# Kernel tuning notes

Hardware: AMD Instinct MI355X
Metric: run time of the kernel (lower is better)

## Reference

```python
import jax, jax.numpy as jnp
import numpy as np
from jax import lax

N, G, L, D, E, STEPS = 65536, 128, 512, 128, 262144, 6
C = 2 * D  # concat dim (input_dim + output_dim)


def setup_inputs() -> dict:
    key = jax.random.key(0)
    ks = jax.random.split(key, 12)
    sD = 1.0 / float(np.sqrt(D))
    sC = 1.0 / float(np.sqrt(C))
    return {
        "x": jax.random.normal(ks[0], (N, D), jnp.float32),
        "edge_index": jax.random.randint(ks[1], (2, E), 0, N, dtype=jnp.int32),
        "edge_weight": jax.random.uniform(ks[2], (E,), jnp.float32),
        "batch": (jnp.arange(N) // L).astype(jnp.int32),  # sorted graph ids, L nodes/graph
        "ggnn_w": jax.random.normal(ks[3], (STEPS, D, D), jnp.float32) * sD,
        "gru_wih": jax.random.normal(ks[4], (3 * D, D), jnp.float32) * sD,
        "gru_whh": jax.random.normal(ks[5], (3 * D, D), jnp.float32) * sD,
        "gru_bih": jnp.zeros((3 * D,), jnp.float32),
        "gru_bhh": jnp.zeros((3 * D,), jnp.float32),
        "conv1_w": jax.random.normal(ks[6], (D, D, 3), jnp.float32) * sD,
        "conv1_b": jnp.zeros((D,), jnp.float32),
        "conv2_w": jax.random.normal(ks[7], (D, D, 1), jnp.float32) * sD,
        "conv2_b": jnp.zeros((D,), jnp.float32),
        "convc1_w": jax.random.normal(ks[8], (C, C, 3), jnp.float32) * sC,
        "convc1_b": jnp.zeros((C,), jnp.float32),
        "convc2_w": jax.random.normal(ks[9], (C, C, 1), jnp.float32) * sC,
        "convc2_b": jnp.zeros((C,), jnp.float32),
        "bn1_g": jnp.ones((D,), jnp.float32),
        "bn1_b": jnp.zeros((D,), jnp.float32),
        "bn2_g": jnp.ones((C,), jnp.float32),
        "bn2_b": jnp.zeros((C,), jnp.float32),
        "mlpy_w": jax.random.normal(ks[10], (2, D), jnp.float32) * sD,
        "mlpy_b": jnp.zeros((2,), jnp.float32),
        "mlpz_w": jax.random.normal(ks[11], (2, C), jnp.float32) * sC,
        "mlpz_b": jnp.zeros((2,), jnp.float32),
    }


def _gru(m, h, wih, whh, bih, bhh):
    gx = m @ wih.T + bih
    gh = h @ whh.T + bhh
    xr, xz, xn = jnp.split(gx, 3, axis=-1)
    hr, hz, hn = jnp.split(gh, 3, axis=-1)
    r = jax.nn.sigmoid(xr + hr)
    z = jax.nn.sigmoid(xz + hz)
    n = jnp.tanh(xn + r * hn)
    return (1.0 - z) * n + z * h


def _conv1d(x, w, b):  # x [G,Cin,L], w [Cout,Cin,K]
    y = lax.conv_general_dilated(x, w, (1,), "VALID", dimension_numbers=("NCH", "OIH", "NCH"))
    return y + b[None, :, None]


def _maxpool(x, k, s):
    return lax.reduce_window(x, -jnp.inf, lax.max, (1, 1, k), (1, 1, s), "VALID")


def _bn(x, g, b):  # training-mode BatchNorm1d over (N, L) per channel
    mean = x.mean(axis=(0, 2), keepdims=True)
    var = x.var(axis=(0, 2), keepdims=True)
    return (x - mean) * lax.rsqrt(var + 1e-5) * g[None, :, None] + b[None, :, None]


def reference(x, edge_index, edge_weight, batch, ggnn_w, gru_wih, gru_whh, gru_bih,
              gru_bhh, conv1_w, conv1_b, conv2_w, conv2_b, convc1_w, convc1_b,
              convc2_w, convc2_b, bn1_g, bn1_b, bn2_g, bn2_b, mlpy_w, mlpy_b,
              mlpz_w, mlpz_b):
    src, dst = edge_index[0], edge_index[1]

    # GatedGraphConv: per layer linear -> weighted message scatter-add -> GRU update
    def step(h, w):
        m = h @ w
        agg = jax.ops.segment_sum(m[src] * edge_weight[:, None], dst, num_segments=N)
        return _gru(agg, h, gru_wih, gru_whh, gru_bih, gru_bhh), None

    h, _ = lax.scan(step, x, ggnn_w)

    # de_batchify_graphs: one fused scatter into zero-padded [G, L, *] tensor
    counts = jax.ops.segment_sum(jnp.ones((N,), jnp.int32), batch, num_segments=G)
    offsets = jnp.cumsum(counts) - counts
    pos = jnp.arange(N) - offsets[batch]
    x_i = jnp.zeros((G, L, D), x.dtype).at[batch, pos].set(x)
    h_i = jnp.zeros((G, L, D), h.dtype).at[batch, pos].set(h)
    c_i = jnp.concatenate([h_i, x_i], axis=-1)  # [G, L, 2D]

    hT = h_i.transpose(0, 2, 1)  # [G, D, L]
    Y1 = _maxpool(jax.nn.relu(_bn(_conv1d(hT, conv1_w, conv1_b), bn1_g, bn1_b)), 3, 2)
    Y2 = _maxpool(jax.nn.relu(_bn(_conv1d(Y1, conv2_w, conv2_b), bn1_g, bn1_b)), 2, 2).transpose(0, 2, 1)
    cT = c_i.transpose(0, 2, 1)  # [G, 2D, L]
    Z1 = _maxpool(jax.nn.relu(_bn(_conv1d(cT, convc1_w, convc1_b), bn2_g, bn2_b)), 3, 2)
    Z2 = _maxpool(jax.nn.relu(_bn(_conv1d(Z1, convc2_w, convc2_b), bn2_g, bn2_b)), 2, 2).transpose(0, 2, 1)

    before_avg = (Y2 @ mlpy_w.T + mlpy_b) * (Z2 @ mlpz_w.T + mlpz_b)  # [G, L', 2]
    return before_avg.mean(axis=1)  # [G, 2]
```

## Files before the change

### kernel.cpp

```cpp
#include <hip/hip_runtime.h>
#include <math.h>

#define NN 65536
#define GG 128
#define LL 512
#define DD 128
#define EE 262144
#define NSTEPS 6
#define CC 256
#define L1 510
#define P1 254
#define P2 127

typedef __attribute__((ext_vector_type(8))) short s8bf;
typedef __attribute__((ext_vector_type(4))) float f4acc;

__device__ __forceinline__ unsigned short f2bf(float x) {
  unsigned u = __float_as_uint(x);
  unsigned r = u + 0x7FFFu + ((u >> 16) & 1u);
  return (unsigned short)(r >> 16);
}
__device__ __forceinline__ float bf2f(unsigned short h) {
  return __uint_as_float(((unsigned)h) << 16);
}
__device__ __forceinline__ unsigned short f2bf_sel(float x, int lo_sel) {
  unsigned short hi = f2bf(x);
  if (!lo_sel) return hi;
  return f2bf(x - bf2f(hi));
}
__device__ __forceinline__ uint2 pack4bf(float4 v, int lo_sel) {
  unsigned short s0 = f2bf_sel(v.x, lo_sel), s1 = f2bf_sel(v.y, lo_sel);
  unsigned short s2 = f2bf_sel(v.z, lo_sel), s3 = f2bf_sel(v.w, lo_sel);
  uint2 pk; pk.x = (unsigned)s0 | ((unsigned)s1 << 16);
  pk.y = (unsigned)s2 | ((unsigned)s3 << 16);
  return pk;
}

__global__ __launch_bounds__(256) void k_prep(
    const float* __restrict__ wih, const float* __restrict__ whh,
    const float* __restrict__ gw,
    const float* __restrict__ w1, const float* __restrict__ wc1,
    const float* __restrict__ w2, const float* __restrict__ wc2,
    unsigned short* __restrict__ wihCh, unsigned short* __restrict__ wihCl,
    unsigned short* __restrict__ whhCh, unsigned short* __restrict__ whhCl,
    unsigned short* __restrict__ gwTh, unsigned short* __restrict__ gwTl,
    unsigned short* __restrict__ c1h, unsigned short* __restrict__ c1l,
    unsigned short* __restrict__ cc1h, unsigned short* __restrict__ cc1l,
    unsigned short* __restrict__ c2h, unsigned short* __restrict__ c2l,
    unsigned short* __restrict__ cc2h, unsigned short* __restrict__ cc2l) {
  int i = blockIdx.x * 256 + threadIdx.x;
  if (i < 49152) {
    float v = wih[i];
    unsigned short h_ = f2bf(v);
    wihCh[i] = h_; wihCl[i] = f2bf(v - bf2f(h_));
    float u = whh[i];
    unsigned short h2 = f2bf(u);
    whhCh[i] = h2; whhCl[i] = f2bf(u - bf2f(h2));
  }
  if (i < 98304) {
    int s = i >> 14; int r = i & 16383; int c = r >> 7; int k = r & 127;
    float v = gw[(s << 14) + k * 128 + c];
    unsigned short h_ = f2bf(v);
    gwTh[i] = h_; gwTl[i] = f2bf(v - bf2f(h_));
  }
  if (i < 49152) {
    int ci = i & 127; int r = i >> 7; int co = r & 127; int tap = r >> 7;
    float v = w1[(co * 128 + ci) * 3 + tap];
    unsigned short h_ = f2bf(v);
    c1h[i] = h_; c1l[i] = f2bf(v - bf2f(h_));
  }
  if (i < 196608) {
    int ci = i & 255; int r = i >> 8; int co = r & 255; int tap = r >> 8;
    float v = wc1[(co * 256 + ci) * 3 + tap];
    unsigned short h_ = f2bf(v);
    cc1h[i] = h_; cc1l[i] = f2bf(v - bf2f(h_));
  }
  if (i < 16384) {
    float v = w2[i];
    unsigned short h_ = f2bf(v);
    c2h[i] = h_; c2l[i] = f2bf(v - bf2f(h_));
  }
  if (i < 65536) {
    float v = wc2[i];
    unsigned short h_ = f2bf(v);
    cc2h[i] = h_; cc2l[i] = f2bf(v - bf2f(h_));
  }
}

__global__ __launch_bounds__(256) void k_hist(const int* __restrict__ dst, int* __restrict__ cnt) {
  int e = blockIdx.x * 256 + threadIdx.x;
  if (e < EE) atomicAdd(&cnt[dst[e]], 1);
}

__global__ __launch_bounds__(1024) void k_scan(const int* __restrict__ cnt,
                                               int* __restrict__ rowptr,
                                               int* __restrict__ cursor) {
  __shared__ int part[1024];
  int t = threadIdx.x;
  int base = t * 64;
  int s = 0;
  for (int i = 0; i < 64; i++) s += cnt[base + i];
  part[t] = s;
  __syncthreads();
  for (int off = 1; off < 1024; off <<= 1) {
    int v = part[t];
    int u = (t >= off) ? part[t - off] : 0;
    __syncthreads();
    part[t] = v + u;
    __syncthreads();
  }
  int run = part[t] - s;
  for (int i = 0; i < 64; i++) {
    rowptr[base + i] = run;
    cursor[base + i] = run;
    run += cnt[base + i];
  }
  if (t == 1023) rowptr[NN] = run;
}

__global__ __launch_bounds__(256) void k_fill(const int* __restrict__ src,
                                              const int* __restrict__ dst,
                                              const float* __restrict__ ew,
                                              int* __restrict__ cursor,
                                              int* __restrict__ col,
                                              float* __restrict__ wgt) {
  int e = blockIdx.x * 256 + threadIdx.x;
  if (e < EE) {
    int d = dst[e];
    int p = atomicAdd(&cursor[d], 1);
    col[p] = src[e];
    wgt[p] = ew[e];
  }
}

__global__ __launch_bounds__(256, 4) void k_gemm_mfma(
    const float* __restrict__ A,
    const unsigned short* __restrict__ Wh, const unsigned short* __restrict__ Wl,
    float* __restrict__ Cout) {
  __shared__ __attribute__((aligned(16))) unsigned short As[64 * 136];
  int t = threadIdx.x;
  int r0 = blockIdx.x * 64;
  int wv = t >> 6, lane = t & 63;
  int ln = lane & 15, q = lane >> 4;
  f4acc acc[4][2];
#pragma unroll
  for (int mt = 0; mt < 4; mt++)
#pragma unroll
    for (int nt = 0; nt < 2; nt++) acc[mt][nt] = (f4acc)0.f;

  for (int p = 0; p < 3; p++) {
    if (p != 1) {
      const int a_lo = (p == 2);
      if (p) __syncthreads();
      for (int base = t * 4; base < 64 * 128; base += 1024) {
        int row = base >> 7, kk = base & 127;
        float4 v = *(const float4*)&A[(r0 + row) * 128 + kk];
        *(uint2*)&As[row * 136 + kk] = pack4bf(v, a_lo);
      }
      __syncthreads();
    }
    const unsigned short* W = (p == 1) ? Wl : Wh;
#pragma unroll
    for (int k0 = 0; k0 < 128; k0 += 32) {
      s8bf af[4], bf[2];
#pragma unroll
      for (int nt = 0; nt < 2; nt++)
        bf[nt] = *(const s8bf*)&W[(wv * 32 + nt * 16 + ln) * 128 + k0 + q * 8];
#pragma unroll
      for (int mt = 0; mt < 4; mt++)
        af[mt] = *(const s8bf*)&As[(mt * 16 + ln) * 136 + k0 + q * 8];
#pragma unroll
      for (int mt = 0; mt < 4; mt++)
#pragma unroll
        for (int nt = 0; nt < 2; nt++)
          acc[mt][nt] = __builtin_amdgcn_mfma_f32_16x16x32_bf16(af[mt], bf[nt], acc[mt][nt], 0, 0, 0);
    }
  }
#pragma unroll
  for (int mt = 0; mt < 4; mt++)
#pragma unroll
    for (int nt = 0; nt < 2; nt++)
#pragma unroll
      for (int reg = 0; reg < 4; reg++) {
        int r = r0 + mt * 16 + q * 4 + reg;
        Cout[r * 128 + wv * 32 + nt * 16 + ln] = acc[mt][nt][reg];
      }
}

__global__ __launch_bounds__(256) void k_gather(const float* __restrict__ m,
                                                const int* __restrict__ rowptr,
                                                const int* __restrict__ col,
                                                const float* __restrict__ wgt,
                                                float* __restrict__ agg) {
  int t = threadIdx.x;
  int n = blockIdx.x * 8 + (t >> 5);
  int c4 = t & 31;
  const float4* m4 = (const float4*)m;
  int s0 = rowptr[n], s1 = rowptr[n + 1];
  float ax = 0.f, ay = 0.f, az = 0.f, aw = 0.f;
  int e = s0;
  for (; e + 2 <= s1; e += 2) {
    int cA = col[e], cB = col[e + 1];
    float wA = wgt[e], wB = wgt[e + 1];
    float4 vA = m4[cA * 32 + c4];
    float4 vB = m4[cB * 32 + c4];
    ax += vA.x * wA + vB.x * wB;
    ay += vA.y * wA + vB.y * wB;
    az += vA.z * wA + vB.z * wB;
    aw += vA.w * wA + vB.w * wB;
  }
  if (e < s1) {
    int cA = col[e];
    float wA = wgt[e];
    float4 vA = m4[cA * 32 + c4];
    ax += vA.x * wA; ay += vA.y * wA; az += vA.z * wA; aw += vA.w * wA;
  }
  ((float4*)agg)[n * 32 + c4] = make_float4(ax, ay, az, aw);
}

__global__ __launch_bounds__(256, 2) void k_gru_mfma(
    const float* __restrict__ agg, const float* __restrict__ hin,
    const unsigned short* __restrict__ wihCh, const unsigned short* __restrict__ wihCl,
    const unsigned short* __restrict__ whhCh, const unsigned short* __restrict__ whhCl,
    const float* __restrict__ bih, const float* __restrict__ bhh,
    float* __restrict__ hout) {
  __shared__ __attribute__((aligned(16))) unsigned short As[2 * 64 * 136];
  int t = threadIdx.x;
  int r0 = blockIdx.x * 64;
  int d0 = blockIdx.y * 64;
  int wv = t >> 6, lane = t & 63;
  int ln = lane & 15, q = lane >> 4;
  f4acc acc[4][6];
#pragma unroll
  for (int mt = 0; mt < 4; mt++)
#pragma unroll
    for (int tg = 0; tg < 6; tg++) acc[mt][tg] = (f4acc)0.f;

  for (int p = 0; p < 3; p++) {
    if (p != 1) {
      const int a_lo = (p == 2);
      if (p) __syncthreads();
#pragma unroll
      for (int mat = 0; mat < 2; mat++) {
        const float* Asrc = mat ? hin : agg;
        for (int base = t * 4; base < 64 * 128; base += 1024) {
          int row = base >> 7, kk = base & 127;
          float4 v = *(const float4*)&Asrc[(r0 + row) * 128 + kk];
          *(uint2*)&As[mat * 8704 + row * 136 + kk] = pack4bf(v, a_lo);
        }
      }
      __syncthreads();
    }
    const unsigned short* wx = (p == 1) ? wihCl : wihCh;
    const unsigned short* wh = (p == 1) ? whhCl : whhCh;
#pragma unroll
    for (int k0 = 0; k0 < 128; k0 += 32) {
      s8bf af[2][4], bfr[6];
#pragma unroll
      for (int tg = 0; tg < 6; tg++) {
        int gate = (tg < 3) ? tg : tg - 3;
        const unsigned short* W = (tg < 3) ? wx : wh;
        bfr[tg] = *(const s8bf*)&W[(gate * 128 + d0 + wv * 16 + ln) * 128 + k0 + q * 8];
      }
#pragma unroll
      for (int mat = 0; mat < 2; mat++)
#pragma unroll
        for (int mt = 0; mt < 4; mt++)
          af[mat][mt] = *(const s8bf*)&As[mat * 8704 + (mt * 16 + ln) * 136 + k0 + q * 8];
#pragma unroll
      for (int mt = 0; mt < 4; mt++)
#pragma unroll
        for (int tg = 0; tg < 6; tg++)
          acc[mt][tg] = __builtin_amdgcn_mfma_f32_16x16x32_bf16(
              af[tg < 3 ? 0 : 1][mt], bfr[tg], acc[mt][tg], 0, 0, 0);
    }
  }
  int d = d0 + wv * 16 + ln;
  float bi0 = bih[d], bi1 = bih[128 + d], bi2 = bih[256 + d];
  float bh0 = bhh[d], bh1 = bhh[128 + d], bh2 = bhh[256 + d];
#pragma unroll
  for (int mt = 0; mt < 4; mt++) {
#pragma unroll
    for (int reg = 0; reg < 4; reg++) {
      int r = r0 + mt * 16 + q * 4 + reg;
      float hold = hin[r * 128 + d];
      float xr = acc[mt][0][reg] + bi0;
      float xz = acc[mt][1][reg] + bi1;
      float xn = acc[mt][2][reg] + bi2;
      float hr = acc[mt][3][reg] + bh0;
      float hz = acc[mt][4][reg] + bh1;
      float hn = acc[mt][5][reg] + bh2;
      float rr = 1.f / (1.f + expf(-(xr + hr)));
      float zz = 1.f / (1.f + expf(-(xz + hz)));
      float nnv = tanhf(xn + rr * hn);
      hout[r * 128 + d] = (1.f - zz) * nnv + zz * hold;
    }
  }
}

template<int CIN, int TAPS, int WA>
__global__ __launch_bounds__(256, 3) void k_conv_mfma(
    const float* __restrict__ inA, const float* __restrict__ inB,
    const unsigned short* __restrict__ Wh, const unsigned short* __restrict__ Wl,
    const float* __restrict__ bias, float* __restrict__ out,
    float* __restrict__ stats, int Lin, int Lco) {
  constexpr int APAD = CIN + 8;
  constexpr int ROWS = 64 + TAPS - 1;
  constexpr int NCH = CIN / 32;
  __shared__ __attribute__((aligned(16))) unsigned short As[ROWS * APAD];
  __shared__ float sred[256];
  const int g = blockIdx.z, co0 = blockIdx.y * 128, l0 = blockIdx.x * 64;
  const int t = threadIdx.x;
  const int wv = t >> 6, lane = t & 63, ln = lane & 15, q = lane >> 4;
  f4acc acc[4][2];
#pragma unroll
  for (int mt = 0; mt < 4; mt++)
#pragma unroll
    for (int nt = 0; nt < 2; nt++) acc[mt][nt] = (f4acc)0.f;

  for (int p = 0; p < 3; p++) {
    if (p != 1) {
      const int a_lo = (p == 2);
      if (p) __syncthreads();
      for (int base = t * 4; base < ROWS * CIN; base += 1024) {
        int row = base / CIN, ch = base % CIN;
        int lr = l0 + row; if (lr > Lin - 1) lr = Lin - 1;
        float4 v;
        if (ch < WA) v = *(const float4*)&inA[(g * Lin + lr) * WA + ch];
        else         v = *(const float4*)&inB[(g * Lin + lr) * WA + ch - WA];
        *(uint2*)&As[row * APAD + ch] = pack4bf(v, a_lo);
      }
      __syncthreads();
    }
    const unsigned short* W = (p == 1) ? Wl : Wh;
#pragma unroll
    for (int tap = 0; tap < TAPS; tap++) {
#pragma unroll
      for (int ch = 0; ch < NCH; ch++) {
        const int c0 = ch * 32;
        s8bf af[4], bf[2];
#pragma unroll
        for (int nt = 0; nt < 2; nt++)
          bf[nt] = *(const s8bf*)&W[(tap * CIN + co0 + wv * 32 + nt * 16 + ln) * CIN + c0 + q * 8];
#pragma unroll
        for (int mt = 0; mt < 4; mt++)
          af[mt] = *(const s8bf*)&As[(mt * 16 + ln + tap) * APAD + c0 + q * 8];
#pragma unroll
        for (int mt = 0; mt < 4; mt++)
#pragma unroll
          for (int nt = 0; nt < 2; nt++)
            acc[mt][nt] = __builtin_amdgcn_mfma_f32_16x16x32_bf16(af[mt], bf[nt], acc[mt][nt], 0, 0, 0);
      }
    }
  }
  sred[t] = 0.f;
  __syncthreads();
#pragma unroll
  for (int nt = 0; nt < 2; nt++) {
    int cl = wv * 32 + nt * 16 + ln;
    int co = co0 + cl;
    float bv = bias[co];
    float s = 0.f, s2 = 0.f;
#pragma unroll
    for (int mt = 0; mt < 4; mt++)
#pragma unroll
      for (int reg = 0; reg < 4; reg++) {
        int l = l0 + mt * 16 + q * 4 + reg;
        if (l < Lco) {
          float v = acc[mt][nt][reg] + bv;
          out[(g * Lco + l) * CIN + co] = v;
          s += v; s2 += v * v;
        }
      }
    atomicAdd(&sred[cl], s);
    atomicAdd(&sred[128 + cl], s2);
  }
  __syncthreads();
  if (t < 128) atomicAdd(&stats[co0 + t], sred[t]);
  else atomicAdd(&stats[CIN + co0 + (t - 128)], sred[t]);
}

__global__ __launch_bounds__(256) void k_bnpool(const float* __restrict__ in,
                                                float* __restrict__ out,
                                                const float* __restrict__ stats,
                                                const float* __restrict__ gamma,
                                                const float* __restrict__ beta,
                                                int Cch, int LinC, int Lout, int pk) {
  int idx = blockIdx.x * 256 + threadIdx.x;
  int total = GG * Cch * Lout;
  if (idx >= total) return;
  int c = idx & (Cch - 1);
  int r = idx / Cch;
  int p = r % Lout;
  int g = r / Lout;
  float cntf = (float)(GG * LinC);
  float mean = stats[c] / cntf;
  float var = stats[Cch + c] / cntf - mean * mean;
  float inv = rsqrtf(var + 1e-5f) * gamma[c];
  float sh = beta[c] - mean * inv;
  const float* base = &in[((g * LinC) + 2 * p) * Cch + c];
  float m = 0.f;
  for (int k = 0; k < pk; k++) {
    float v = fmaxf(base[k * Cch] * inv + sh, 0.f);
    m = fmaxf(m, v);
  }
  out[(g * Lout + p) * Cch + c] = m;
}

__global__ __launch_bounds__(128) void k_final(const float* __restrict__ Y2,
                                               const float* __restrict__ Z2,
                                               const float* __restrict__ myw,
                                               const float* __restrict__ myb,
                                               const float* __restrict__ mzw,
                                               const float* __restrict__ mzb,
                                               float* __restrict__ outp) {
  __shared__ float red0[128];
  __shared__ float red1[128];
  int g = blockIdx.x;
  int t = threadIdx.x;
  float y0 = myb[0], y1 = myb[1], z0 = mzb[0], z1 = mzb[1];
  if (t < P2) {
    const float* yb = &Y2[(g * P2 + t) * 128];
    for (int c = 0; c < 128; c++) {
      float v = yb[c];
      y0 += v * myw[c];
      y1 += v * myw[128 + c];
    }
    const float* zb = &Z2[(g * P2 + t) * 256];
    for (int c = 0; c < 256; c++) {
      float v = zb[c];
      z0 += v * mzw[c];
      z1 += v * mzw[256 + c];
    }
  }
  red0[t] = (t < P2) ? y0 * z0 : 0.f;
  red1[t] = (t < P2) ? y1 * z1 : 0.f;
  __syncthreads();
  for (int off = 64; off > 0; off >>= 1) {
    if (t < off) {
      red0[t] += red0[t + off];
      red1[t] += red1[t + off];
    }
    __syncthreads();
  }
  if (t == 0) {
    outp[g * 2 + 0] = red0[0] / 127.f;
    outp[g * 2 + 1] = red1[0] / 127.f;
  }
}

extern "C" void kernel_launch(void* const* d_in, const int* in_sizes, int n_in,
                              void* d_out, int out_size, void* d_ws, size_t ws_size,
                              hipStream_t stream) {
  const float* x   = (const float*)d_in[0];
  const int* ei    = (const int*)d_in[1];
  const float* ew  = (const float*)d_in[2];
  const float* gw  = (const float*)d_in[4];
  const float* wih = (const float*)d_in[5];
  const float* whh = (const float*)d_in[6];
  const float* bih = (const float*)d_in[7];
  const float* bhh = (const float*)d_in[8];
  const float* w1  = (const float*)d_in[9];
  const float* b1  = (const float*)d_in[10];
  const float* w2  = (const float*)d_in[11];
  const float* b2  = (const float*)d_in[12];
  const float* wc1 = (const float*)d_in[13];
  const float* bc1 = (const float*)d_in[14];
  const float* wc2 = (const float*)d_in[15];
  const float* bc2 = (const float*)d_in[16];
  const float* bn1g = (const float*)d_in[17];
  const float* bn1b = (const float*)d_in[18];
  const float* bn2g = (const float*)d_in[19];
  const float* bn2b = (const float*)d_in[20];
  const float* myw = (const float*)d_in[21];
  const float* myb = (const float*)d_in[22];
  const float* mzw = (const float*)d_in[23];
  const float* mzb = (const float*)d_in[24];
  float* out = (float*)d_out;

  float* ws   = (float*)d_ws;
  float* h    = ws;
  float* bufA = h + 8388608;
  float* bufB = bufA + 16711680;
  float* bufC = bufB + 8388608;
  float* Y2   = bufC + 8388608;
  float* Z2   = Y2 + 2080768;
  float* wslot = Z2 + 4161536;
  unsigned short* wihCh = (unsigned short*)wslot;
  unsigned short* wihCl = wihCh + 49152;
  unsigned short* whhCh = wihCl + 49152;
  unsigned short* whhCl = whhCh + 49152;
  unsigned short* c1h  = (unsigned short*)(wslot + 98304);
  unsigned short* c1l  = c1h + 49152;
  unsigned short* cc1h = c1l + 49152;
  unsigned short* cc1l = cc1h + 196608;
  unsigned short* c2h  = cc1l + 196608;
  unsigned short* c2l  = c2h + 16384;
  unsigned short* cc2h = c2l + 16384;
  unsigned short* cc2l = cc2h + 65536;
  float* stats = (float*)(cc2l + 65536);
  int* cnt    = (int*)(stats + 512);
  int* rowptr = cnt + 65536;
  int* cursor = rowptr + 65537;
  int* col    = cursor + 65536;
  float* wgt  = (float*)(col + 262144);
  unsigned short* gwTh = (unsigned short*)(wgt + 262144);
  unsigned short* gwTl = gwTh + 98304;
  size_t needed = (size_t)((float*)(gwTl + 98304) - ws) * 4;
  if (ws_size < needed) return;

  const int* src = ei;
  const int* dst = ei + EE;

  k_prep<<<768, 256, 0, stream>>>(wih, whh, gw, w1, wc1, w2, wc2,
                                  wihCh, wihCl, whhCh, whhCl, gwTh, gwTl,
                                  c1h, c1l, cc1h, cc1l, c2h, c2l, cc2h, cc2l);
  hipMemsetAsync(cnt, 0, 65536 * 4, stream);
  k_hist<<<1024, 256, 0, stream>>>(dst, cnt);
  k_scan<<<1, 1024, 0, stream>>>(cnt, rowptr, cursor);
  k_fill<<<1024, 256, 0, stream>>>(src, dst, ew, cursor, col, wgt);

  float* P = h;
  float* Q = bufC;
  float* m = bufA;
  float* agg = bufB;
  for (int s = 0; s < NSTEPS; s++) {
    const float* hcur = (s == 0) ? x : ((s & 1) ? Q : P);
    float* hnext = (s & 1) ? P : Q;
    k_gemm_mfma<<<1024, 256, 0, stream>>>(hcur, gwTh + s * 16384, gwTl + s * 16384, m);
    k_gather<<<8192, 256, 0, stream>>>(m, rowptr, col, wgt, agg);
    k_gru_mfma<<<dim3(1024, 2), 256, 0, stream>>>(agg, hcur, wihCh, wihCl,
                                                  whhCh, whhCl, bih, bhh, hnext);
  }

  hipMemsetAsync(stats, 0, 512 * 4, stream);
  k_conv_mfma<128, 3, 128><<<dim3(8, 1, 128), 256, 0, stream>>>(
      h, nullptr, c1h, c1l, b1, bufA, stats, 512, L1);
  k_bnpool<<<(GG * 128 * P1 + 255) / 256, 256, 0, stream>>>(bufA, bufB, stats, bn1g, bn1b, 128, L1, P1, 3);
  hipMemsetAsync(stats, 0, 512 * 4, stream);
  k_conv_mfma<128, 1, 128><<<dim3(4, 1, 128), 256, 0, stream>>>(
      bufB, nullptr, c2h, c2l, b2, bufC, stats, P1, P1);
  k_bnpool<<<(GG * 128 * P2 + 255) / 256, 256, 0, stream>>>(bufC, Y2, stats, bn1g, bn1b, 128, P1, P2, 2);

  hipMemsetAsync(stats, 0, 512 * 4, stream);
  k_conv_mfma<256, 3, 128><<<dim3(8, 2, 128), 256, 0, stream>>>(
      h, x, cc1h, cc1l, bc1, bufA, stats, 512, L1);
  k_bnpool<<<(GG * 256 * P1 + 255) / 256, 256, 0, stream>>>(bufA, bufB, stats, bn2g, bn2b, 256, L1, P1, 3);
  hipMemsetAsync(stats, 0, 512 * 4, stream);
  k_conv_mfma<256, 1, 256><<<dim3(4, 2, 128), 256, 0, stream>>>(
      bufB, nullptr, cc2h, cc2l, bc2, bufC, stats, P1, P1);
  k_bnpool<<<(GG * 256 * P2 + 255) / 256, 256, 0, stream>>>(bufC, Z2, stats, bn2g, bn2b, 256, P1, P2, 2);

  k_final<<<128, 128, 0, stream>>>(Y2, Z2, myw, myb, mzw, mzb, out);
}
```

Before: 1.648 ms.

## Store activations as split bf16 hi/lo planes instead of fp32 across pipeline

```diff
diff --git a/kernel.cpp b/kernel.cpp
--- a/kernel.cpp
+++ b/kernel.cpp
@@ -87,6 +87,21 @@
   }
 }
 
+__global__ __launch_bounds__(256) void k_castx(const float* __restrict__ x,
+                                               unsigned short* __restrict__ xH,
+                                               unsigned short* __restrict__ xL) {
+  int i = blockIdx.x * 256 + threadIdx.x;
+  const float4* x4 = (const float4*)x;
+  float4 a = x4[i * 2 + 0];
+  float4 b = x4[i * 2 + 1];
+  uint2 ha = pack4bf(a, 0), hb = pack4bf(b, 0);
+  uint2 la = pack4bf(a, 1), lb = pack4bf(b, 1);
+  uint4 hv; hv.x = ha.x; hv.y = ha.y; hv.z = hb.x; hv.w = hb.y;
+  uint4 lv; lv.x = la.x; lv.y = la.y; lv.z = lb.x; lv.w = lb.y;
+  *(uint4*)&xH[i * 8] = hv;
+  *(uint4*)&xL[i * 8] = lv;
+}
+
 __global__ __launch_bounds__(256) void k_hist(const int* __restrict__ dst, int* __restrict__ cnt) {
   int e = blockIdx.x * 256 + threadIdx.x;
   if (e < EE) atomicAdd(&cnt[dst[e]], 1);
@@ -134,7 +149,7 @@
 }
 
 __global__ __launch_bounds__(256, 4) void k_gemm_mfma(
-    const float* __restrict__ A,
+    const unsigned short* __restrict__ Ah, const unsigned short* __restrict__ Al,
     const unsigned short* __restrict__ Wh, const unsigned short* __restrict__ Wl,
     float* __restrict__ Cout) {
   __shared__ __attribute__((aligned(16))) unsigned short As[64 * 136];
@@ -150,12 +165,13 @@
 
   for (int p = 0; p < 3; p++) {
     if (p != 1) {
-      const int a_lo = (p == 2);
+      const unsigned short* S = (p == 2) ? Al : Ah;
       if (p) __syncthreads();
-      for (int base = t * 4; base < 64 * 128; base += 1024) {
-        int row = base >> 7, kk = base & 127;
-        float4 v = *(const float4*)&A[(r0 + row) * 128 + kk];
-        *(uint2*)&As[row * 136 + kk] = pack4bf(v, a_lo);
+#pragma unroll
+      for (int it = 0; it < 4; it++) {
+        int v8 = it * 256 + t;
+        int row = v8 >> 4, k = (v8 & 15) * 8;
+        *(uint4*)&As[row * 136 + k] = *(const uint4*)&S[(r0 + row) * 128 + k];
       }
       __syncthreads();
     }
@@ -191,7 +207,8 @@
                                                 const int* __restrict__ rowptr,
                                                 const int* __restrict__ col,
                                                 const float* __restrict__ wgt,
-                                                float* __restrict__ agg) {
+                                                unsigned short* __restrict__ aggH,
+                                                unsigned short* __restrict__ aggL) {
   int t = threadIdx.x;
   int n = blockIdx.x * 8 + (t >> 5);
   int c4 = t & 31;
@@ -215,15 +232,24 @@
     float4 vA = m4[cA * 32 + c4];
     ax += vA.x * wA; ay += vA.y * wA; az += vA.z * wA; aw += vA.w * wA;
   }
-  ((float4*)agg)[n * 32 + c4] = make_float4(ax, ay, az, aw);
+  unsigned short h0 = f2bf(ax), h1 = f2bf(ay), h2 = f2bf(az), h3 = f2bf(aw);
+  unsigned short l0 = f2bf(ax - bf2f(h0)), l1 = f2bf(ay - bf2f(h1));
+  unsigned short l2 = f2bf(az - bf2f(h2)), l3 = f2bf(aw - bf2f(h3));
+  uint2 hpk, lpk;
+  hpk.x = (unsigned)h0 | ((unsigned)h1 << 16); hpk.y = (unsigned)h2 | ((unsigned)h3 << 16);
+  lpk.x = (unsigned)l0 | ((unsigned)l1 << 16); lpk.y = (unsigned)l2 | ((unsigned)l3 << 16);
+  int base = n * 128 + c4 * 4;
+  *(uint2*)&aggH[base] = hpk;
+  *(uint2*)&aggL[base] = lpk;
 }
 
 __global__ __launch_bounds__(256, 2) void k_gru_mfma(
-    const float* __restrict__ agg, const float* __restrict__ hin,
+    const unsigned short* __restrict__ aggH, const unsigned short* __restrict__ aggL,
+    const unsigned short* __restrict__ hinH, const unsigned short* __restrict__ hinL,
     const unsigned short* __restrict__ wihCh, const unsigned short* __restrict__ wihCl,
     const unsigned short* __restrict__ whhCh, const unsigned short* __restrict__ whhCl,
     const float* __restrict__ bih, const float* __restrict__ bhh,
-    float* __restrict__ hout) {
+    unsigned short* __restrict__ houtH, unsigned short* __restrict__ houtL) {
   __shared__ __attribute__((aligned(16))) unsigned short As[2 * 64 * 136];
   int t = threadIdx.x;
   int r0 = blockIdx.x * 64;
@@ -238,16 +264,16 @@
 
   for (int p = 0; p < 3; p++) {
     if (p != 1) {
-      const int a_lo = (p == 2);
+      const unsigned short* s0 = (p == 2) ? aggL : aggH;
+      const unsigned short* s1 = (p == 2) ? hinL : hinH;
       if (p) __syncthreads();
 #pragma unroll
-      for (int mat = 0; mat < 2; mat++) {
-        const float* Asrc = mat ? hin : agg;
-        for (int base = t * 4; base < 64 * 128; base += 1024) {
-          int row = base >> 7, kk = base & 127;
-          float4 v = *(const float4*)&Asrc[(r0 + row) * 128 + kk];
-          *(uint2*)&As[mat * 8704 + row * 136 + kk] = pack4bf(v, a_lo);
-        }
+      for (int it = 0; it < 8; it++) {
+        int v8 = it * 256 + t;
+        int mat = v8 >> 10;
+        int row = (v8 >> 4) & 63, k = (v8 & 15) * 8;
+        const unsigned short* S = mat ? s1 : s0;
+        *(uint4*)&As[mat * 8704 + row * 136 + k] = *(const uint4*)&S[(r0 + row) * 128 + k];
       }
       __syncthreads();
     }
@@ -283,7 +309,8 @@
 #pragma unroll
     for (int reg = 0; reg < 4; reg++) {
       int r = r0 + mt * 16 + q * 4 + reg;
-      float hold = hin[r * 128 + d];
+      int idx = r * 128 + d;
+      float hold = bf2f(hinH[idx]) + bf2f(hinL[idx]);
       float xr = acc[mt][0][reg] + bi0;
       float xz = acc[mt][1][reg] + bi1;
       float xn = acc[mt][2][reg] + bi2;
@@ -293,20 +320,27 @@
       float rr = 1.f / (1.f + expf(-(xr + hr)));
       float zz = 1.f / (1.f + expf(-(xz + hz)));
       float nnv = tanhf(xn + rr * hn);
-      hout[r * 128 + d] = (1.f - zz) * nnv + zz * hold;
+      float hv = (1.f - zz) * nnv + zz * hold;
+      unsigned short hh = f2bf(hv);
+      houtH[idx] = hh;
+      houtL[idx] = f2bf(hv - bf2f(hh));
     }
   }
 }
 
 template<int CIN, int TAPS, int WA>
-__global__ __launch_bounds__(256, 3) void k_conv_mfma(
-    const float* __restrict__ inA, const float* __restrict__ inB,
+__global__ __launch_bounds__(256, 4) void k_conv_mfma(
+    const unsigned short* __restrict__ hiA, const unsigned short* __restrict__ hiB,
+    const unsigned short* __restrict__ loA, const unsigned short* __restrict__ loB,
     const unsigned short* __restrict__ Wh, const unsigned short* __restrict__ Wl,
     const float* __restrict__ bias, float* __restrict__ out,
     float* __restrict__ stats, int Lin, int Lco) {
   constexpr int APAD = CIN + 8;
   constexpr int ROWS = 64 + TAPS - 1;
   constexpr int NCH = CIN / 32;
+  constexpr int TOT8 = ROWS * CIN / 8;
+  constexpr int NIT = (TOT8 + 255) / 256;
+  constexpr int NINNER = TAPS * NCH;
   __shared__ __attribute__((aligned(16))) unsigned short As[ROWS * APAD];
   __shared__ float sred[256];
   const int g = blockIdx.z, co0 = blockIdx.y * 128, l0 = blockIdx.x * 64;
@@ -320,37 +354,48 @@
 
   for (int p = 0; p < 3; p++) {
     if (p != 1) {
-      const int a_lo = (p == 2);
+      const unsigned short* pA = (p == 2) ? loA : hiA;
+      const unsigned short* pB = (p == 2) ? loB : hiB;
       if (p) __syncthreads();
-      for (int base = t * 4; base < ROWS * CIN; base += 1024) {
-        int row = base / CIN, ch = base % CIN;
-        int lr = l0 + row; if (lr > Lin - 1) lr = Lin - 1;
-        float4 v;
-        if (ch < WA) v = *(const float4*)&inA[(g * Lin + lr) * WA + ch];
-        else         v = *(const float4*)&inB[(g * Lin + lr) * WA + ch - WA];
-        *(uint2*)&As[row * APAD + ch] = pack4bf(v, a_lo);
+#pragma unroll
+      for (int it = 0; it < NIT; it++) {
+        int v8 = it * 256 + t;
+        if (NIT * 256 == TOT8 || v8 < TOT8) {
+          int row = (v8 * 8) / CIN, ch = (v8 * 8) % CIN;
+          int lr = l0 + row; if (lr > Lin - 1) lr = Lin - 1;
+          uint4 v;
+          if (ch < WA) v = *(const uint4*)&pA[(g * Lin + lr) * WA + ch];
+          else         v = *(const uint4*)&pB[(g * Lin + lr) * WA + ch - WA];
+          *(uint4*)&As[row * APAD + ch] = v;
+        }
       }
       __syncthreads();
     }
     const unsigned short* W = (p == 1) ? Wl : Wh;
-#pragma unroll
-    for (int tap = 0; tap < TAPS; tap++) {
-#pragma unroll
-      for (int ch = 0; ch < NCH; ch++) {
-        const int c0 = ch * 32;
-        s8bf af[4], bf[2];
+    s8bf bcur[2], bnxt[2];
+#pragma unroll
+    for (int nt = 0; nt < 2; nt++)
+      bcur[nt] = *(const s8bf*)&W[(co0 + wv * 32 + nt * 16 + ln) * CIN + q * 8];
+#pragma unroll
+    for (int it = 0; it < NINNER; it++) {
+      const int tap = it / NCH, ch = it % NCH;
+      if (it + 1 < NINNER) {
+        const int ntap = (it + 1) / NCH, nch = (it + 1) % NCH;
 #pragma unroll
         for (int nt = 0; nt < 2; nt++)
-          bf[nt] = *(const s8bf*)&W[(tap * CIN + co0 + wv * 32 + nt * 16 + ln) * CIN + c0 + q * 8];
-#pragma unroll
-        for (int mt = 0; mt < 4; mt++)
-          af[mt] = *(const s8bf*)&As[(mt * 16 + ln + tap) * APAD + c0 + q * 8];
-#pragma unroll
-        for (int mt = 0; mt < 4; mt++)
-#pragma unroll
-          for (int nt = 0; nt < 2; nt++)
-            acc[mt][nt] = __builtin_amdgcn_mfma_f32_16x16x32_bf16(af[mt], bf[nt], acc[mt][nt], 0, 0, 0);
+          bnxt[nt] = *(const s8bf*)&W[(ntap * CIN + co0 + wv * 32 + nt * 16 + ln) * CIN + nch * 32 + q * 8];
       }
+      const int c0 = ch * 32;
+      s8bf af[4];
+#pragma unroll
+      for (int mt = 0; mt < 4; mt++)
+        af[mt] = *(const s8bf*)&As[(mt * 16 + ln + tap) * APAD + c0 + q * 8];
+#pragma unroll
+      for (int mt = 0; mt < 4; mt++)
+#pragma unroll
+        for (int nt = 0; nt < 2; nt++)
+          acc[mt][nt] = __builtin_amdgcn_mfma_f32_16x16x32_bf16(af[mt], bcur[nt], acc[mt][nt], 0, 0, 0);
+      if (it + 1 < NINNER) { bcur[0] = bnxt[0]; bcur[1] = bnxt[1]; }
     }
   }
   sred[t] = 0.f;
@@ -380,8 +425,11 @@
   else atomicAdd(&stats[CIN + co0 + (t - 128)], sred[t]);
 }
 
+template<bool PLANES>
 __global__ __launch_bounds__(256) void k_bnpool(const float* __restrict__ in,
-                                                float* __restrict__ out,
+                                                float* __restrict__ outF,
+                                                unsigned short* __restrict__ outH,
+                                                unsigned short* __restrict__ outL,
                                                 const float* __restrict__ stats,
                                                 const float* __restrict__ gamma,
                                                 const float* __restrict__ beta,
@@ -404,7 +452,14 @@
     float v = fmaxf(base[k * Cch] * inv + sh, 0.f);
     m = fmaxf(m, v);
   }
-  out[(g * Lout + p) * Cch + c] = m;
+  int o = (g * Lout + p) * Cch + c;
+  if (PLANES) {
+    unsigned short hh = f2bf(m);
+    outH[o] = hh;
+    outL[o] = f2bf(m - bf2f(hh));
+  } else {
+    outF[o] = m;
+  }
 }
 
 __global__ __launch_bounds__(128) void k_final(const float* __restrict__ Y2,
@@ -478,19 +533,12 @@
   const float* mzb = (const float*)d_in[24];
   float* out = (float*)d_out;
 
-  float* ws   = (float*)d_ws;
-  float* h    = ws;
-  float* bufA = h + 8388608;
-  float* bufB = bufA + 16711680;
-  float* bufC = bufB + 8388608;
-  float* Y2   = bufC + 8388608;
-  float* Z2   = Y2 + 2080768;
-  float* wslot = Z2 + 4161536;
-  unsigned short* wihCh = (unsigned short*)wslot;
-  unsigned short* wihCl = wihCh + 49152;
-  unsigned short* whhCh = wihCl + 49152;
-  unsigned short* whhCl = whhCh + 49152;
-  unsigned short* c1h  = (unsigned short*)(wslot + 98304);
+  float* ws = (float*)d_ws;
+  unsigned short* PH = (unsigned short*)ws;
+  unsigned short* PL = PH + 8388608;
+  unsigned short* xH = PL + 8388608;
+  unsigned short* xL = xH + 8388608;
+  unsigned short* c1h  = xL + 8388608;
   unsigned short* c1l  = c1h + 49152;
   unsigned short* cc1h = c1l + 49152;
   unsigned short* cc1l = cc1h + 196608;
@@ -499,14 +547,32 @@
   unsigned short* cc2h = c2l + 16384;
   unsigned short* cc2l = cc2h + 65536;
   float* stats = (float*)(cc2l + 65536);
-  int* cnt    = (int*)(stats + 512);
+  float* Y2 = stats + 512;
+  float* Z2 = Y2 + 2080768;
+  float* shared0 = Z2 + 4161536;
+  unsigned short* QH = (unsigned short*)shared0;
+  unsigned short* QL = QH + 8388608;
+  float* m = (float*)(QL + 8388608);
+  unsigned short* aggH = (unsigned short*)(m + 8388608);
+  unsigned short* aggL = aggH + 8388608;
+  unsigned short* wihCh = aggL + 8388608;
+  unsigned short* wihCl = wihCh + 49152;
+  unsigned short* whhCh = wihCl + 49152;
+  unsigned short* whhCl = whhCh + 49152;
+  unsigned short* gwTh = whhCl + 49152;
+  unsigned short* gwTl = gwTh + 98304;
+  int* cnt    = (int*)(gwTl + 98304);
   int* rowptr = cnt + 65536;
   int* cursor = rowptr + 65537;
   int* col    = cursor + 65536;
   float* wgt  = (float*)(col + 262144);
-  unsigned short* gwTh = (unsigned short*)(wgt + 262144);
-  unsigned short* gwTl = gwTh + 98304;
-  size_t needed = (size_t)((float*)(gwTl + 98304) - ws) * 4;
+  float* ggnn_end = wgt + 262144;
+  float* bufA = shared0;
+  unsigned short* bufBH = (unsigned short*)(bufA + 16711680);
+  unsigned short* bufBL = bufBH + 8323072;
+  float* conv_end = (float*)(bufBL + 8323072);
+  float* wend = (ggnn_end > conv_end) ? ggnn_end : conv_end;
+  size_t needed = (size_t)(wend - ws) * 4;
   if (ws_size < needed) return;
 
   const int* src = ei;
@@ -515,41 +581,44 @@
   k_prep<<<768, 256, 0, stream>>>(wih, whh, gw, w1, wc1, w2, wc2,
                                   wihCh, wihCl, whhCh, whhCl, gwTh, gwTl,
                                   c1h, c1l, cc1h, cc1l, c2h, c2l, cc2h, cc2l);
+  k_castx<<<4096, 256, 0, stream>>>(x, xH, xL);
   hipMemsetAsync(cnt, 0, 65536 * 4, stream);
   k_hist<<<1024, 256, 0, stream>>>(dst, cnt);
   k_scan<<<1, 1024, 0, stream>>>(cnt, rowptr, cursor);
   k_fill<<<1024, 256, 0, stream>>>(src, dst, ew, cursor, col, wgt);
 
-  float* P = h;
-  float* Q = bufC;
-  float* m = bufA;
-  float* agg = bufB;
   for (int s = 0; s < NSTEPS; s++) {
-    const float* hcur = (s == 0) ? x : ((s & 1) ? Q : P);
-    float* hnext = (s & 1) ? P : Q;
-    k_gemm_mfma<<<1024, 256, 0, stream>>>(hcur, gwTh + s * 16384, gwTl + s * 16384, m);
-    k_gather<<<8192, 256, 0, stream>>>(m, rowptr, col, wgt, agg);
-    k_gru_mfma<<<dim3(1024, 2), 256, 0, stream>>>(agg, hcur, wihCh, wihCl,
-                                                  whhCh, whhCl, bih, bhh, hnext);
+    const unsigned short* AH = (s == 0) ? xH : ((s & 1) ? QH : PH);
+    const unsigned short* AL = (s == 0) ? xL : ((s & 1) ? QL : PL);
+    unsigned short* OH = (s & 1) ? PH : QH;
+    unsigned short* OL = (s & 1) ? PL : QL;
+    k_gemm_mfma<<<1024, 256, 0, stream>>>(AH, AL, gwTh + s * 16384, gwTl + s * 16384, m);
+    k_gather<<<8192, 256, 0, stream>>>(m, rowptr, col, wgt, aggH, aggL);
+    k_gru_mfma<<<dim3(1024, 2), 256, 0, stream>>>(aggH, aggL, AH, AL, wihCh, wihCl,
+                                                  whhCh, whhCl, bih, bhh, OH, OL);
   }
 
   hipMemsetAsync(stats, 0, 512 * 4, stream);
   k_conv_mfma<128, 3, 128><<<dim3(8, 1, 128), 256, 0, stream>>>(
-      h, nullptr, c1h, c1l, b1, bufA, stats, 512, L1);
-  k_bnpool<<<(GG * 128 * P1 + 255) / 256, 256, 0, stream>>>(bufA, bufB, stats, bn1g, bn1b, 128, L1, P1, 3);
+      PH, nullptr, PL, nullptr, c1h, c1l, b1, bufA, stats, 512, L1);
+  k_bnpool<true><<<(GG * 128 * P1 + 255) / 256, 256, 0, stream>>>(
+      bufA, nullptr, bufBH, bufBL, stats, bn1g, bn1b, 128, L1, P1, 3);
   hipMemsetAsync(stats, 0, 512 * 4, stream);
   k_conv_mfma<128, 1, 128><<<dim3(4, 1, 128), 256, 0, stream>>>(
-      bufB, nullptr, c2h, c2l, b2, bufC, stats, P1, P1);
-  k_bnpool<<<(GG * 128 * P2 + 255) / 256, 256, 0, stream>>>(bufC, Y2, stats, bn1g, bn1b, 128, P1, P2, 2);
+      bufBH, nullptr, bufBL, nullptr, c2h, c2l, b2, bufA, stats, P1, P1);
+  k_bnpool<false><<<(GG * 128 * P2 + 255) / 256, 256, 0, stream>>>(
+      bufA, Y2, nullptr, nullptr, stats, bn1g, bn1b, 128, P1, P2, 2);
 
   hipMemsetAsync(stats, 0, 512 * 4, stream);
   k_conv_mfma<256, 3, 128><<<dim3(8, 2, 128), 256, 0, stream>>>(
-      h, x, cc1h, cc1l, bc1, bufA, stats, 512, L1);
-  k_bnpool<<<(GG * 256 * P1 + 255) / 256, 256, 0, stream>>>(bufA, bufB, stats, bn2g, bn2b, 256, L1, P1, 3);
+      PH, xH, PL, xL, cc1h, cc1l, bc1, bufA, stats, 512, L1);
+  k_bnpool<true><<<(GG * 256 * P1 + 255) / 256, 256, 0, stream>>>(
+      bufA, nullptr, bufBH, bufBL, stats, bn2g, bn2b, 256, L1, P1, 3);
   hipMemsetAsync(stats, 0, 512 * 4, stream);
   k_conv_mfma<256, 1, 256><<<dim3(4, 2, 128), 256, 0, stream>>>(
-      bufB, nullptr, cc2h, cc2l, bc2, bufC, stats, P1, P1);
-  k_bnpool<<<(GG * 256 * P2 + 255) / 256, 256, 0, stream>>>(bufC, Z2, stats, bn2g, bn2b, 256, P1, P2, 2);
+      bufBH, nullptr, bufBL, nullptr, cc2h, cc2l, bc2, bufA, stats, P1, P1);
+  k_bnpool<false><<<(GG * 256 * P2 + 255) / 256, 256, 0, stream>>>(
+      bufA, Z2, nullptr, nullptr, stats, bn2g, bn2b, 256, P1, P2, 2);
 
   k_final<<<128, 128, 0, stream>>>(Y2, Z2, myw, myb, mzw, mzb, out);
 }
```

Result: faster. 1.580 ms (-4.1%).
